# Optimization experiments

Measured on AMD Instinct MI355X. Metric: run time of the kernel, lower is better.

The kernel has to match this reference:

```python
import jax, jax.numpy as jnp
import numpy as np

DIM = 256
HEADS = 8
WIN = (2, 7, 7)
BW = 512
NW = 64  # num windows (mask leading dim); BW % NW == 0


def _relative_position_index(win):
    Wz, Wh, Ww = win
    coords = np.stack(np.meshgrid(np.arange(Wz), np.arange(Wh), np.arange(Ww), indexing='ij'))
    cf = coords.reshape(3, -1)  # (3, N)
    rel = cf[:, :, None] - cf[:, None, :]  # (3, N, N)
    rel = rel.transpose(1, 2, 0).copy()
    rel[:, :, 0] += Wz - 1
    rel[:, :, 1] += Wh - 1
    rel[:, :, 2] += Ww - 1
    rel[:, :, 0] *= (2 * Wh - 1) * (2 * Ww - 1)
    rel[:, :, 1] *= 2 * Ww - 1
    return rel.sum(-1).astype(np.int32)  # (N, N)


def setup_inputs() -> dict:
    key = jax.random.key(0)
    ks = jax.random.split(key, 8)
    N = WIN[0] * WIN[1] * WIN[2]
    table_size = (2 * WIN[0] - 1) * (2 * WIN[1] - 1) * (2 * WIN[2] - 1)
    return {
        'x': jax.random.normal(ks[0], (BW, N, DIM), dtype=jnp.float32),
        'qkv_w': jax.random.normal(ks[1], (DIM, 3 * DIM), dtype=jnp.float32) * 0.02,
        'qkv_b': jax.random.normal(ks[2], (3 * DIM,), dtype=jnp.float32) * 0.02,
        'bias_table': jax.random.normal(ks[3], (table_size, HEADS), dtype=jnp.float32) * 0.02,
        'proj_w': jax.random.normal(ks[4], (DIM, DIM), dtype=jnp.float32) * 0.02,
        'proj_b': jax.random.normal(ks[5], (DIM,), dtype=jnp.float32) * 0.02,
        'mask': jax.random.normal(ks[6], (NW, N, N), dtype=jnp.float32),
        'rpi': jnp.asarray(_relative_position_index(WIN)),
    }


def reference(x, qkv_w, qkv_b, bias_table, proj_w, proj_b, mask, rpi):
    BW_, N, C = x.shape
    H = HEADS
    D = C // H
    scale = D ** (-0.5)
    # qkv projection -> (3, BW, H, N, D)
    qkv = (x @ qkv_w + qkv_b).reshape(BW_, N, 3, H, D).transpose(2, 0, 3, 1, 4)
    q, k, v = qkv[0], qkv[1], qkv[2]
    attn = jnp.einsum('bhnd,bhmd->bhnm', q * scale, k)  # (BW, H, N, N)
    # relative position bias gather: (N, N, H) -> (H, N, N)
    bias = bias_table[rpi.reshape(-1)].reshape(N, N, H).transpose(2, 0, 1)
    attn = attn + bias[None]
    nW = mask.shape[0]
    attn = attn.reshape(BW_ // nW, nW, H, N, N) + mask[None, :, None]
    attn = attn.reshape(BW_, H, N, N)
    attn = jax.nn.softmax(attn, axis=-1)
    out = jnp.einsum('bhnm,bhmd->bhnd', attn, v)
    out = out.transpose(0, 2, 1, 3).reshape(BW_, N, C)
    return out @ proj_w + proj_b
```

## Files before the change

kernel.cpp:

```cpp
#include <hip/hip_runtime.h>
#include <math.h>

typedef short bf8v __attribute__((ext_vector_type(8)));
typedef float f32x4 __attribute__((ext_vector_type(4)));

#define SCALE 0.17677669529663687f

__device__ __forceinline__ unsigned short f2bf(float f) {
    union { float f; unsigned int u; } c; c.f = f;
    unsigned int r = (c.u + 0x7FFFu + ((c.u >> 16) & 1u)) >> 16;
    return (unsigned short)r;
}

__device__ __forceinline__ int sw32(int row, int k8) {
    return row * 32 + ((k8 ^ ((row >> 1) & 3)) << 3);
}
__device__ __forceinline__ int sw128(int row, int c8) {
    return row * 128 + (((c8 ^ row) & 15) << 3);
}
__device__ __forceinline__ int bidx(int row, int col) {
    return row * 128 + ((((col >> 3) ^ (((row >> 2) & 3) << 1)) & 15) << 3) + (col & 7);
}

__global__ __launch_bounds__(256) void cvt_x_kernel(const float* __restrict__ in,
                                                    unsigned short* __restrict__ out, int n8) {
    int i = blockIdx.x * 256 + threadIdx.x;
    if (i >= n8) return;
    const float4* p = (const float4*)(in + (size_t)i * 8);
    float4 a = p[0], b = p[1];
    union { int4 v; unsigned short u[8]; } o;
    o.u[0]=f2bf(a.x); o.u[1]=f2bf(a.y); o.u[2]=f2bf(a.z); o.u[3]=f2bf(a.w);
    o.u[4]=f2bf(b.x); o.u[5]=f2bf(b.y); o.u[6]=f2bf(b.z); o.u[7]=f2bf(b.w);
    *(int4*)(out + (size_t)i * 8) = o.v;
}

__global__ __launch_bounds__(256) void tcvt_w_kernel(const float* __restrict__ in,
                                                     unsigned short* __restrict__ out, int C) {
    int idx = blockIdx.x * 256 + threadIdx.x;
    int c = idx >> 8, r = idx & 255;
    if (c < C) out[idx] = f2bf(in[r * C + c]);
}

__global__ __launch_bounds__(256) void bm_kernel(const float* __restrict__ bias_table,
                                                 const int* __restrict__ rpi,
                                                 const float* __restrict__ mask,
                                                 float* __restrict__ bm) {
    int bx = blockIdx.x;
    int w = bx >> 3, h = bx & 7;
    const float* mp = mask + (size_t)w * 9604;
    float* op = bm + (size_t)bx * 9604;
    for (int e = threadIdx.x; e < 9604; e += 256)
        op[e] = bias_table[rpi[e] * 8 + h] + mp[e];
}

__global__ __launch_bounds__(256) void qkv_gemm_kernel(
    const unsigned short* __restrict__ A, const unsigned short* __restrict__ B,
    const float* __restrict__ bias, unsigned short* __restrict__ qkv)
{
    __shared__ unsigned short As[128 * 32];
    __shared__ unsigned short Bs[128 * 32];
    __shared__ unsigned short Cb[128 * 128];
    const int tid = threadIdx.x;
    const int lane = tid & 63, wid = tid >> 6;
    const int l16 = lane & 15, lg = lane >> 4;
    const int wr = wid >> 1, wc = wid & 1;
    const int nb = (blockIdx.x & 7) * 294 + (blockIdx.x >> 3);
    const int bm0 = (nb / 6) * 128, bn0 = (nb % 6) * 128;

    f32x4 acc[4][4] = {};
    const int crow = tid >> 2, ck8 = tid & 3;

    for (int k0 = 0; k0 < 256; k0 += 32) {
        __syncthreads();
        *(int4*)&As[sw32(crow,      ck8)] = *(const int4*)(A + (size_t)(bm0 + crow     ) * 256 + k0 + ck8 * 8);
        *(int4*)&As[sw32(crow + 64, ck8)] = *(const int4*)(A + (size_t)(bm0 + crow + 64) * 256 + k0 + ck8 * 8);
        *(int4*)&Bs[sw32(crow,      ck8)] = *(const int4*)(B + (size_t)(bn0 + crow     ) * 256 + k0 + ck8 * 8);
        *(int4*)&Bs[sw32(crow + 64, ck8)] = *(const int4*)(B + (size_t)(bn0 + crow + 64) * 256 + k0 + ck8 * 8);
        __syncthreads();
        bf8v af[4], bfr[4];
        #pragma unroll
        for (int mt = 0; mt < 4; ++mt) af[mt]  = *(const bf8v*)&As[sw32(wr*64 + mt*16 + l16, lg)];
        #pragma unroll
        for (int nt = 0; nt < 4; ++nt) bfr[nt] = *(const bf8v*)&Bs[sw32(wc*64 + nt*16 + l16, lg)];
        #pragma unroll
        for (int mt = 0; mt < 4; ++mt)
            #pragma unroll
            for (int nt = 0; nt < 4; ++nt)
                acc[mt][nt] = __builtin_amdgcn_mfma_f32_16x16x32_bf16(af[mt], bfr[nt], acc[mt][nt], 0, 0, 0);
    }

    #pragma unroll
    for (int nt = 0; nt < 4; ++nt) {
        const int colg = bn0 + wc * 64 + nt * 16 + l16;
        const float bv = bias[colg];
        const float sc = (colg < 256) ? SCALE : 1.0f;
        #pragma unroll
        for (int mt = 0; mt < 4; ++mt)
            #pragma unroll
            for (int r = 0; r < 4; ++r) {
                const int rl = wr * 64 + mt * 16 + lg * 4 + r;
                Cb[bidx(rl, wc * 64 + nt * 16 + l16)] = f2bf((acc[mt][nt][r] + bv) * sc);
            }
    }
    __syncthreads();
    #pragma unroll
    for (int c0 = 0; c0 < 8; ++c0) {
        const int c = c0 * 256 + tid;
        const int row = c >> 4, c8 = c & 15;
        const int4 val = *(const int4*)&Cb[row * 128 + (((c8 ^ (((row >> 2) & 3) << 1)) & 15) << 3)];
        *(int4*)(qkv + (size_t)(bm0 + row) * 768 + bn0 + c8 * 8) = val;
    }
}

__global__ __launch_bounds__(448) void attn_kernel(
    const unsigned short* __restrict__ qkv, const float* __restrict__ bm,
    unsigned short* __restrict__ att)
{
    __shared__ unsigned short Qs[112 * 32];
    __shared__ unsigned short Ks[112 * 32];
    __shared__ unsigned short Vt[32 * 128];
    __shared__ unsigned short Ps[112 * 128];

    const int nb = (blockIdx.x & 7) * 512 + (blockIdx.x >> 3);
    const int b = nb >> 3, h = nb & 7;
    const int tid = threadIdx.x;
    const int wid = tid >> 6, lane = tid & 63;
    const int l16 = lane & 15, lg = lane >> 4;
    const unsigned short* base = qkv + (size_t)b * 98 * 768 + h * 32;

    if (tid < 392) {
        const int row = tid >> 2, k8 = tid & 3;
        const unsigned short* rp = base + (size_t)row * 768 + k8 * 8;
        *(int4*)&Qs[sw32(row, k8)] = *(const int4*)(rp);
        *(int4*)&Ks[sw32(row, k8)] = *(const int4*)(rp + 256);
        union { int4 v; unsigned short u[8]; } t;
        t.v = *(const int4*)(rp + 512);
        #pragma unroll
        for (int j = 0; j < 8; ++j) {
            const int d = k8 * 8 + j;
            Vt[sw128(d, row >> 3) + (row & 7)] = t.u[j];
        }
    } else {
        const int t2 = tid - 392;
        const int row = 98 + (t2 >> 2), k8 = t2 & 3;
        const int4 z = {0, 0, 0, 0};
        *(int4*)&Qs[sw32(row, k8)] = z;
        *(int4*)&Ks[sw32(row, k8)] = z;
    }
    for (int e = tid; e < 32 * 30; e += 448) {
        const int d = e / 30, n = 98 + e - (e / 30) * 30;
        Vt[sw128(d, n >> 3) + (n & 7)] = 0;
    }
    __syncthreads();

    const int rt = wid;
    const bf8v qf = *(const bf8v*)&Qs[sw32(rt * 16 + l16, lg)];
    f32x4 sa[7];
    const f32x4 zero = {0.f, 0.f, 0.f, 0.f};
    #pragma unroll
    for (int ct = 0; ct < 7; ++ct) {
        const bf8v kf = *(const bf8v*)&Ks[sw32(ct * 16 + l16, lg)];
        sa[ct] = __builtin_amdgcn_mfma_f32_16x16x32_bf16(qf, kf, zero, 0, 0, 0);
    }

    const float* bmp = bm + (size_t)((b & 63) * 8 + h) * 9604;
    #pragma unroll
    for (int ct = 0; ct < 7; ++ct) {
        const int col = ct * 16 + l16;
        const int colc = col < 98 ? col : 97;
        #pragma unroll
        for (int r = 0; r < 4; ++r) {
            const int row = rt * 16 + lg * 4 + r;
            const int rowc = row < 98 ? row : 97;
            const float add = bmp[rowc * 98 + colc];
            sa[ct][r] = (col < 98) ? (sa[ct][r] + add) : -INFINITY;
        }
    }

    #pragma unroll
    for (int r = 0; r < 4; ++r) {
        float mx = sa[0][r];
        #pragma unroll
        for (int ct = 1; ct < 7; ++ct) mx = fmaxf(mx, sa[ct][r]);
        #pragma unroll
        for (int off = 1; off < 16; off <<= 1) mx = fmaxf(mx, __shfl_xor(mx, off));
        float sum = 0.f;
        #pragma unroll
        for (int ct = 0; ct < 7; ++ct) { const float e = __expf(sa[ct][r] - mx); sa[ct][r] = e; sum += e; }
        #pragma unroll
        for (int off = 1; off < 16; off <<= 1) sum += __shfl_xor(sum, off);
        const float inv = 1.0f / sum;
        const int row = rt * 16 + lg * 4 + r;
        #pragma unroll
        for (int ct = 0; ct < 7; ++ct) {
            const int col = ct * 16 + l16;
            Ps[sw128(row, col >> 3) + (col & 7)] = f2bf(sa[ct][r] * inv);
        }
    }
    #pragma unroll
    for (int e0 = 0; e0 < 4; ++e0) {
        const int e = e0 * 64 + lane;
        const int row = rt * 16 + (e >> 4), col = 112 + (e & 15);
        Ps[sw128(row, col >> 3) + (col & 7)] = 0;
    }

    f32x4 oacc[2] = {};
    #pragma unroll
    for (int ks = 0; ks < 4; ++ks) {
        const bf8v pf = *(const bf8v*)&Ps[sw128(rt * 16 + l16, ks * 4 + lg)];
        #pragma unroll
        for (int dt = 0; dt < 2; ++dt) {
            const bf8v vf = *(const bf8v*)&Vt[sw128(dt * 16 + l16, ks * 4 + lg)];
            oacc[dt] = __builtin_amdgcn_mfma_f32_16x16x32_bf16(pf, vf, oacc[dt], 0, 0, 0);
        }
    }

    #pragma unroll
    for (int r = 0; r < 4; ++r) {
        const int row = rt * 16 + lg * 4 + r;
        if (row < 98) {
            #pragma unroll
            for (int dt = 0; dt < 2; ++dt)
                att[((size_t)b * 98 + row) * 256 + h * 32 + dt * 16 + l16] = f2bf(oacc[dt][r]);
        }
    }
}

__global__ __launch_bounds__(256) void proj_gemm_kernel(
    const unsigned short* __restrict__ A, const unsigned short* __restrict__ B,
    const float* __restrict__ pb, float* __restrict__ out)
{
    __shared__ unsigned short As[128 * 32];
    __shared__ unsigned short Bs[128 * 32];
    const int tid = threadIdx.x;
    const int lane = tid & 63, wid = tid >> 6;
    const int l16 = lane & 15, lg = lane >> 4;
    const int wr = wid >> 1, wc = wid & 1;
    const int nb = (blockIdx.x & 7) * 98 + (blockIdx.x >> 3);
    const int bm0 = (nb >> 1) * 128, bn0 = (nb & 1) * 128;

    f32x4 acc[4][4] = {};
    const int crow = tid >> 2, ck8 = tid & 3;

    for (int k0 = 0; k0 < 256; k0 += 32) {
        __syncthreads();
        *(int4*)&As[sw32(crow,      ck8)] = *(const int4*)(A + (size_t)(bm0 + crow     ) * 256 + k0 + ck8 * 8);
        *(int4*)&As[sw32(crow + 64, ck8)] = *(const int4*)(A + (size_t)(bm0 + crow + 64) * 256 + k0 + ck8 * 8);
        *(int4*)&Bs[sw32(crow,      ck8)] = *(const int4*)(B + (size_t)(bn0 + crow     ) * 256 + k0 + ck8 * 8);
        *(int4*)&Bs[sw32(crow + 64, ck8)] = *(const int4*)(B + (size_t)(bn0 + crow + 64) * 256 + k0 + ck8 * 8);
        __syncthreads();
        bf8v af[4], bfr[4];
        #pragma unroll
        for (int mt = 0; mt < 4; ++mt) af[mt]  = *(const bf8v*)&As[sw32(wr*64 + mt*16 + l16, lg)];
        #pragma unroll
        for (int nt = 0; nt < 4; ++nt) bfr[nt] = *(const bf8v*)&Bs[sw32(wc*64 + nt*16 + l16, lg)];
        #pragma unroll
        for (int mt = 0; mt < 4; ++mt)
            #pragma unroll
            for (int nt = 0; nt < 4; ++nt)
                acc[mt][nt] = __builtin_amdgcn_mfma_f32_16x16x32_bf16(af[mt], bfr[nt], acc[mt][nt], 0, 0, 0);
    }

    #pragma unroll
    for (int mt = 0; mt < 4; ++mt)
        #pragma unroll
        for (int r = 0; r < 4; ++r) {
            const int row = bm0 + wr*64 + mt*16 + lg*4 + r;
            #pragma unroll
            for (int nt = 0; nt < 4; ++nt) {
                const int col = bn0 + wc*64 + nt*16 + l16;
                out[(size_t)row * 256 + col] = acc[mt][nt][r] + pb[col];
            }
        }
}

extern "C" void kernel_launch(void* const* d_in, const int* in_sizes, int n_in,
                              void* d_out, int out_size, void* d_ws, size_t ws_size,
                              hipStream_t stream) {
    const float* x          = (const float*)d_in[0];
    const float* qkv_w      = (const float*)d_in[1];
    const float* qkv_b      = (const float*)d_in[2];
    const float* bias_table = (const float*)d_in[3];
    const float* proj_w     = (const float*)d_in[4];
    const float* proj_b     = (const float*)d_in[5];
    const float* mask       = (const float*)d_in[6];
    const int*   rpi        = (const int*)d_in[7];
    float* out = (float*)d_out;

    const size_t SEG = (size_t)50176 * 256;
    unsigned short* xb   = (unsigned short*)d_ws;
    unsigned short* wtq  = xb + SEG;
    unsigned short* wtp  = wtq + 768 * 256;
    unsigned short* qkvb = wtp + 256 * 256;
    unsigned short* attb = qkvb + 3 * SEG;
    float* bm = (float*)(attb + SEG);

    cvt_x_kernel<<<6272, 256, 0, stream>>>(x, xb, (int)(SEG / 8));
    tcvt_w_kernel<<<768, 256, 0, stream>>>(qkv_w, wtq, 768);
    tcvt_w_kernel<<<256, 256, 0, stream>>>(proj_w, wtp, 256);
    bm_kernel<<<512, 256, 0, stream>>>(bias_table, rpi, mask, bm);

    qkv_gemm_kernel<<<2352, 256, 0, stream>>>(xb, wtq, qkv_b, qkvb);
    attn_kernel<<<4096, 448, 0, stream>>>(qkvb, bm, attb);
    proj_gemm_kernel<<<784, 256, 0, stream>>>(attb, wtp, proj_b, out);
}
```

Baseline: 262.8 us.

## Fuse x bf16 conversion into QKV GEMM, pad bias-mask, regroup attention blocks

Removes the standalone x-to-bf16 conversion pass by converting fp32 x while loading A tiles inside the QKV GEMM. The two weight-transpose launches become one. The bias+mask table is pre-padded to 112x112 with -1e30 for padded columns, which drops the clamping and select logic in attention. Attention blocks are remapped so blocks sharing a mask window land on the same XCD, and shared memory is aliased (Ps over Qs/Ks) behind an added barrier. The trade-off is twice the fp32 A-tile global reads in the GEMM and reconverting x for each of the 6 column tiles.

```diff
diff --git a/kernel.cpp b/kernel.cpp
--- a/kernel.cpp
+++ b/kernel.cpp
@@ -22,23 +22,19 @@
     return row * 128 + ((((col >> 3) ^ (((row >> 2) & 3) << 1)) & 15) << 3) + (col & 7);
 }
 
-__global__ __launch_bounds__(256) void cvt_x_kernel(const float* __restrict__ in,
-                                                    unsigned short* __restrict__ out, int n8) {
-    int i = blockIdx.x * 256 + threadIdx.x;
-    if (i >= n8) return;
-    const float4* p = (const float4*)(in + (size_t)i * 8);
-    float4 a = p[0], b = p[1];
-    union { int4 v; unsigned short u[8]; } o;
-    o.u[0]=f2bf(a.x); o.u[1]=f2bf(a.y); o.u[2]=f2bf(a.z); o.u[3]=f2bf(a.w);
-    o.u[4]=f2bf(b.x); o.u[5]=f2bf(b.y); o.u[6]=f2bf(b.z); o.u[7]=f2bf(b.w);
-    *(int4*)(out + (size_t)i * 8) = o.v;
-}
-
-__global__ __launch_bounds__(256) void tcvt_w_kernel(const float* __restrict__ in,
-                                                     unsigned short* __restrict__ out, int C) {
+__global__ __launch_bounds__(256) void tcvt_w_kernel(const float* __restrict__ w1,
+                                                     const float* __restrict__ w2,
+                                                     unsigned short* __restrict__ wtq,
+                                                     unsigned short* __restrict__ wtp) {
     int idx = blockIdx.x * 256 + threadIdx.x;
-    int c = idx >> 8, r = idx & 255;
-    if (c < C) out[idx] = f2bf(in[r * C + c]);
+    if (idx < 768 * 256) {
+        int c = idx >> 8, r = idx & 255;
+        wtq[idx] = f2bf(w1[r * 768 + c]);
+    } else {
+        int i2 = idx - 768 * 256;
+        int c = i2 >> 8, r = i2 & 255;
+        wtp[i2] = f2bf(w2[r * 256 + c]);
+    }
 }
 
 __global__ __launch_bounds__(256) void bm_kernel(const float* __restrict__ bias_table,
@@ -48,13 +44,22 @@
     int bx = blockIdx.x;
     int w = bx >> 3, h = bx & 7;
     const float* mp = mask + (size_t)w * 9604;
-    float* op = bm + (size_t)bx * 9604;
-    for (int e = threadIdx.x; e < 9604; e += 256)
-        op[e] = bias_table[rpi[e] * 8 + h] + mp[e];
+    float* op = bm + (size_t)bx * 12544;
+    int t = threadIdx.x;
+    if (t >= 224) return;
+    int r0 = (t >= 112) ? 1 : 0;
+    int col = t - 112 * r0;
+    for (int row = r0; row < 112; row += 2) {
+        float val;
+        if (col >= 98)      val = -1e30f;
+        else if (row >= 98) val = 0.0f;
+        else                val = bias_table[rpi[row * 98 + col] * 8 + h] + mp[row * 98 + col];
+        op[row * 112 + col] = val;
+    }
 }
 
 __global__ __launch_bounds__(256) void qkv_gemm_kernel(
-    const unsigned short* __restrict__ A, const unsigned short* __restrict__ B,
+    const float* __restrict__ x, const unsigned short* __restrict__ B,
     const float* __restrict__ bias, unsigned short* __restrict__ qkv)
 {
     __shared__ unsigned short As[128 * 32];
@@ -72,8 +77,16 @@
 
     for (int k0 = 0; k0 < 256; k0 += 32) {
         __syncthreads();
-        *(int4*)&As[sw32(crow,      ck8)] = *(const int4*)(A + (size_t)(bm0 + crow     ) * 256 + k0 + ck8 * 8);
-        *(int4*)&As[sw32(crow + 64, ck8)] = *(const int4*)(A + (size_t)(bm0 + crow + 64) * 256 + k0 + ck8 * 8);
+        #pragma unroll
+        for (int rr = 0; rr < 2; ++rr) {
+            const float* xp = x + (size_t)(bm0 + crow + rr * 64) * 256 + k0 + ck8 * 8;
+            const float4 a0 = *(const float4*)xp;
+            const float4 a1 = *(const float4*)(xp + 4);
+            union { int4 v; unsigned short u[8]; } o;
+            o.u[0]=f2bf(a0.x); o.u[1]=f2bf(a0.y); o.u[2]=f2bf(a0.z); o.u[3]=f2bf(a0.w);
+            o.u[4]=f2bf(a1.x); o.u[5]=f2bf(a1.y); o.u[6]=f2bf(a1.z); o.u[7]=f2bf(a1.w);
+            *(int4*)&As[sw32(crow + rr * 64, ck8)] = o.v;
+        }
         *(int4*)&Bs[sw32(crow,      ck8)] = *(const int4*)(B + (size_t)(bn0 + crow     ) * 256 + k0 + ck8 * 8);
         *(int4*)&Bs[sw32(crow + 64, ck8)] = *(const int4*)(B + (size_t)(bn0 + crow + 64) * 256 + k0 + ck8 * 8);
         __syncthreads();
@@ -116,13 +129,16 @@
     const unsigned short* __restrict__ qkv, const float* __restrict__ bm,
     unsigned short* __restrict__ att)
 {
-    __shared__ unsigned short Qs[112 * 32];
-    __shared__ unsigned short Ks[112 * 32];
-    __shared__ unsigned short Vt[32 * 128];
-    __shared__ unsigned short Ps[112 * 128];
-
-    const int nb = (blockIdx.x & 7) * 512 + (blockIdx.x >> 3);
-    const int b = nb >> 3, h = nb & 7;
+    __shared__ unsigned short SH[18432];
+    unsigned short* Qs = SH;
+    unsigned short* Ks = SH + 3584;
+    unsigned short* Ps = SH;
+    unsigned short* Vt = SH + 14336;
+
+    const int xcd = blockIdx.x & 7, i = blockIdx.x >> 3;
+    const int j = i & 7, h = (i >> 3) & 7, wlo = i >> 6;
+    const int w = xcd * 8 + wlo;
+    const int b = (j << 6) + w;
     const int tid = threadIdx.x;
     const int wid = tid >> 6, lane = tid & 63;
     const int l16 = lane & 15, lg = lane >> 4;
@@ -136,9 +152,9 @@
         union { int4 v; unsigned short u[8]; } t;
         t.v = *(const int4*)(rp + 512);
         #pragma unroll
-        for (int j = 0; j < 8; ++j) {
-            const int d = k8 * 8 + j;
-            Vt[sw128(d, row >> 3) + (row & 7)] = t.u[j];
+        for (int jj = 0; jj < 8; ++jj) {
+            const int d = k8 * 8 + jj;
+            Vt[sw128(d, row >> 3) + (row & 7)] = t.u[jj];
         }
     } else {
         const int t2 = tid - 392;
@@ -163,19 +179,18 @@
         sa[ct] = __builtin_amdgcn_mfma_f32_16x16x32_bf16(qf, kf, zero, 0, 0, 0);
     }
 
-    const float* bmp = bm + (size_t)((b & 63) * 8 + h) * 9604;
+    const float* bmp = bm + (size_t)(w * 8 + h) * 12544;
     #pragma unroll
     for (int ct = 0; ct < 7; ++ct) {
         const int col = ct * 16 + l16;
-        const int colc = col < 98 ? col : 97;
         #pragma unroll
         for (int r = 0; r < 4; ++r) {
             const int row = rt * 16 + lg * 4 + r;
-            const int rowc = row < 98 ? row : 97;
-            const float add = bmp[rowc * 98 + colc];
-            sa[ct][r] = (col < 98) ? (sa[ct][r] + add) : -INFINITY;
-        }
-    }
+            sa[ct][r] += bmp[row * 112 + col];
+        }
+    }
+
+    __syncthreads();
 
     #pragma unroll
     for (int r = 0; r < 4; ++r) {
@@ -288,19 +303,16 @@
     float* out = (float*)d_out;
 
     const size_t SEG = (size_t)50176 * 256;
-    unsigned short* xb   = (unsigned short*)d_ws;
-    unsigned short* wtq  = xb + SEG;
+    unsigned short* wtq  = (unsigned short*)d_ws;
     unsigned short* wtp  = wtq + 768 * 256;
     unsigned short* qkvb = wtp + 256 * 256;
     unsigned short* attb = qkvb + 3 * SEG;
     float* bm = (float*)(attb + SEG);
 
-    cvt_x_kernel<<<6272, 256, 0, stream>>>(x, xb, (int)(SEG / 8));
-    tcvt_w_kernel<<<768, 256, 0, stream>>>(qkv_w, wtq, 768);
-    tcvt_w_kernel<<<256, 256, 0, stream>>>(proj_w, wtp, 256);
+    tcvt_w_kernel<<<1024, 256, 0, stream>>>(qkv_w, proj_w, wtq, wtp);
     bm_kernel<<<512, 256, 0, stream>>>(bias_table, rpi, mask, bm);
 
-    qkv_gemm_kernel<<<2352, 256, 0, stream>>>(xb, wtq, qkv_b, qkvb);
+    qkv_gemm_kernel<<<2352, 256, 0, stream>>>(x, wtq, qkv_b, qkvb);
     attn_kernel<<<4096, 448, 0, stream>>>(qkvb, bm, attb);
     proj_gemm_kernel<<<784, 256, 0, stream>>>(attb, wtp, proj_b, out);
 }
```

Measured after the change: 263.6 us. About the same (+0.3%).
